# Optimization experiments

Measured on AMD Instinct MI355X. Metric: run time of the kernel, lower is better.

Reference implementation:

```python
import jax, jax.numpy as jnp
import numpy as np

H, I, E, TOPK = 2048, 1408, 8, 2
B, S = 2, 2048


def setup_inputs() -> dict:
    key = jax.random.key(0)
    k1, k2, k3, k4, k5 = jax.random.split(key, 5)
    x = jax.random.normal(k1, (B, S, H), dtype=jnp.float32)
    expert_indices = jax.random.randint(k2, (B, S, TOPK), 0, E, dtype=jnp.int64)
    expert_weights = jax.random.uniform(k3, (B, S, TOPK), dtype=jnp.float32)
    # params: w13 = concat([gate, up], dim=1) -> [E, 2I, H]; down_proj [E, H, I]
    w13 = jax.random.normal(k4, (E, 2 * I, H), dtype=jnp.float32) * 0.02
    down_proj = jax.random.normal(k5, (E, H, I), dtype=jnp.float32) * 0.02
    return {"x": x, "expert_indices": expert_indices, "expert_weights": expert_weights,
            "w13": w13, "down_proj": down_proj}


def _moe(x, expert_indices, expert_weights, w13, down_proj):
    b, s, h = x.shape
    T = b * s
    x_flat = x.reshape(T, h)
    idx = expert_indices.reshape(T, -1)            # [T, top_k]
    wts = expert_weights.reshape(T, -1)            # [T, top_k]
    # dense combine weights: routing[t, e] = sum of weights of slots routed to e
    # (matches original scatter/index_add combine, including duplicate experts)
    routing = jnp.zeros((T, w13.shape[0]), x.dtype).at[
        jnp.arange(T)[:, None], idx].add(wts)      # [T, E]
    # per-expert SwiGLU MLP computed densely, zeroed out by routing weights
    gu = jnp.einsum('th,eih->tei', x_flat, w13)    # [T, E, 2I]
    g, u = jnp.split(gu, 2, axis=-1)
    hact = jax.nn.silu(g) * u                      # [T, E, I]
    y = jnp.einsum('tei,ehi->teh', hact, down_proj)  # [T, E, H]
    out = jnp.einsum('te,teh->th', routing, y)     # [T, H]
    return out.reshape(b, s, h)


def reference(x, expert_indices, expert_weights, w13, down_proj):
    return _moe(x, expert_indices, expert_weights, w13, down_proj)
```

## Files before the change

### kernel.cpp

```cpp
#include <hip/hip_runtime.h>
#include <hip/hip_bf16.h>


typedef __bf16 bf16;
typedef bf16 bf16x8 __attribute__((ext_vector_type(8)));
typedef float f32x4 __attribute__((ext_vector_type(4)));

constexpr int Hdim = 2048;
constexpr int Idim = 1408;
constexpr int NE = 8;
constexpr int TOPK = 2;
constexpr int NT = 4096;
constexpr int NPAIR = 8192;
constexpr int BK = 64;

#define GLOAD16(G, L) __builtin_amdgcn_global_load_lds(                    \
    (const __attribute__((address_space(1))) void*)(G),                    \
    (__attribute__((address_space(3))) void*)(L), 16, 0, 0)


__global__ void k_cvt(const float* __restrict__ src, bf16* __restrict__ dst, int n8) {
    int i = blockIdx.x * 256 + threadIdx.x;
    if (i >= n8) return;
    f32x4 a = *reinterpret_cast<const f32x4*>(src + (size_t)i * 8);
    f32x4 b = *reinterpret_cast<const f32x4*>(src + (size_t)i * 8 + 4);
    bf16x8 v;
#pragma unroll
    for (int j = 0; j < 4; j++) { v[j] = (bf16)a[j]; v[4 + j] = (bf16)b[j]; }
    *reinterpret_cast<bf16x8*>(dst + (size_t)i * 8) = v;
}


__global__ void k_bin1(const int* __restrict__ eidx, int* __restrict__ chunkhist) {
    __shared__ int h[NE];
    int t = threadIdx.x;
    if (t < NE) h[t] = 0;
    __syncthreads();
    int p = blockIdx.x * 256 + t;
    atomicAdd(&h[eidx[p]], 1);
    __syncthreads();
    if (t < NE) chunkhist[blockIdx.x * NE + t] = h[t];
}

__global__ void k_bin2(int* __restrict__ meta, const int* __restrict__ chunkhist,
                       int* __restrict__ chunkbase) {
    if (threadIdx.x == 0) {
        int counts[NE];
        for (int e = 0; e < NE; e++) counts[e] = 0;
        for (int b = 0; b < 32; b++)
            for (int e = 0; e < NE; e++) {
                chunkbase[b * NE + e] = counts[e];
                counts[e] += chunkhist[b * NE + e];
            }
        int acc = 0;
        for (int e = 0; e < NE; e++) {
            meta[e] = counts[e];
            meta[8 + e] = acc;
            acc += counts[e];
        }
    }
}

__global__ void k_bin3(const int* __restrict__ eidx, const float* __restrict__ wts,
                       const int* __restrict__ meta, const int* __restrict__ chunkbase,
                       int* __restrict__ token_id, float* __restrict__ weightv) {
    __shared__ int earr[256];
    int t = threadIdx.x;
    int p = blockIdx.x * 256 + t;
    int e = eidx[p];
    earr[t] = e;
    __syncthreads();
    int rank = 0;
    for (int q = 0; q < t; q++) rank += (earr[q] == e) ? 1 : 0;
    int pos = meta[8 + e] + chunkbase[blockIdx.x * NE + e] + rank;
    token_id[pos] = p / TOPK;
    weightv[pos] = wts[p];
}


__global__ __launch_bounds__(256, 2) void k_gemm1(
    const bf16* __restrict__ xb, const bf16* __restrict__ w13b,
    const int* __restrict__ meta, bf16* __restrict__ hact) {
    const int flat = blockIdx.x;
    const int work = (flat & 7) * 176 + (flat >> 3);
    const int mslot = work & 15;
    const int grp = work >> 4;
    const int e = grp / 11;
    const int ytile = grp - e * 11;

    const int n_e = meta[e];
    const int m0 = mslot * 128;
    if (m0 >= n_e) return;
    const int base = meta[8 + e];
    const int* toks = (const int*)(meta + 64) + base;
    const bf16* wg = w13b + (size_t)e * (2 * Idim) * Hdim + (size_t)(ytile * 128) * Hdim;
    const bf16* wu = wg + (size_t)Idim * Hdim;

    __shared__ bf16 As[128 * 64];
    __shared__ bf16 Bg[128 * 64];
    __shared__ bf16 Bu[128 * 64];

    const int tid = threadIdx.x;
    const int lane = tid & 63;
    const int wid = tid >> 6;
    const int wr = wid >> 1, wc = wid & 1;
    const int l16 = lane & 15, lq = lane >> 4;

    const bf16* gA[4];
    const bf16* gG[4];
    const bf16* gU[4];
    int lo[4];
#pragma unroll
    for (int r = 0; r < 4; r++) {
        int sid = r * 256 + tid;
        int row = sid >> 3, seg = sid & 7;
        int ss = seg ^ (row & 7);
        lo[r] = (r * 256 + (tid & ~63)) * 16;
        int rr = m0 + row;
        if (rr >= n_e) rr = n_e - 1;
        gA[r] = xb + (size_t)toks[rr] * Hdim + ss * 8;
        gG[r] = wg + (size_t)row * Hdim + ss * 8;
        gU[r] = wu + (size_t)row * Hdim + ss * 8;
    }

    f32x4 accg[4][4], accu[4][4];
#pragma unroll
    for (int m = 0; m < 4; m++)
#pragma unroll
        for (int n = 0; n < 4; n++) {
            accg[m][n] = f32x4{0.f, 0.f, 0.f, 0.f};
            accu[m][n] = f32x4{0.f, 0.f, 0.f, 0.f};
        }

    for (int k0 = 0; k0 < Hdim; k0 += BK) {
        __syncthreads();
#pragma unroll
        for (int r = 0; r < 4; r++) {
            GLOAD16(gA[r] + k0, (char*)As + lo[r]);
            GLOAD16(gG[r] + k0, (char*)Bg + lo[r]);
            GLOAD16(gU[r] + k0, (char*)Bu + lo[r]);
        }
        __syncthreads();
#pragma unroll
        for (int kk = 0; kk < 2; ++kk) {
            bf16x8 af[4], bgf[4], buf_[4];
#pragma unroll
            for (int m = 0; m < 4; m++) {
                int row = wr * 64 + m * 16 + l16;
                int s = (kk * 4 + lq) ^ (row & 7);
                af[m] = *reinterpret_cast<const bf16x8*>(&As[row * 64 + s * 8]);
            }
#pragma unroll
            for (int n = 0; n < 4; n++) {
                int row = wc * 64 + n * 16 + l16;
                int s = (kk * 4 + lq) ^ (row & 7);
                bgf[n] = *reinterpret_cast<const bf16x8*>(&Bg[row * 64 + s * 8]);
                buf_[n] = *reinterpret_cast<const bf16x8*>(&Bu[row * 64 + s * 8]);
            }
#pragma unroll
            for (int m = 0; m < 4; m++)
#pragma unroll
                for (int n = 0; n < 4; n++) {
                    accg[m][n] = __builtin_amdgcn_mfma_f32_16x16x32_bf16(af[m], bgf[n], accg[m][n], 0, 0, 0);
                    accu[m][n] = __builtin_amdgcn_mfma_f32_16x16x32_bf16(af[m], buf_[n], accu[m][n], 0, 0, 0);
                }
        }
    }

    const int colbase = ytile * 128 + wc * 64;
#pragma unroll
    for (int m = 0; m < 4; m++) {
        int lr0 = m0 + wr * 64 + m * 16 + lq * 4;
#pragma unroll
        for (int j = 0; j < 4; j++) {
            int lr = lr0 + j;
            if (lr < n_e) {
                size_t rowoff = (size_t)(base + lr) * Idim;
#pragma unroll
                for (int n = 0; n < 4; n++) {
                    float g = accg[m][n][j], u = accu[m][n][j];
                    float v = (g / (1.f + __expf(-g))) * u;
                    hact[rowoff + colbase + n * 16 + l16] = (bf16)v;
                }
            }
        }
    }
}


__global__ __launch_bounds__(256, 2) void k_gemm2(
    const bf16* __restrict__ hact, const bf16* __restrict__ dpb,
    const int* __restrict__ meta, const float* __restrict__ weightv,
    float* __restrict__ out) {
    const int flat = blockIdx.x;
    const int work = (flat & 7) * 256 + (flat >> 3);
    const int mslot = work & 15;
    const int grp = work >> 4;
    const int e = grp >> 4;
    const int ytile = grp & 15;

    const int n_e = meta[e];
    const int m0 = mslot * 128;
    if (m0 >= n_e) return;
    const int base = meta[8 + e];
    const int* toks = (const int*)(meta + 64) + base;
    const bf16* wb = dpb + (size_t)e * Hdim * Idim + (size_t)(ytile * 128) * Idim;

    __shared__ bf16 As[128 * 64];
    __shared__ bf16 Bs[128 * 64];

    const int tid = threadIdx.x;
    const int lane = tid & 63;
    const int wid = tid >> 6;
    const int wr = wid >> 1, wc = wid & 1;
    const int l16 = lane & 15, lq = lane >> 4;

    const bf16* gA[4];
    const bf16* gB[4];
    int lo[4];
#pragma unroll
    for (int r = 0; r < 4; r++) {
        int sid = r * 256 + tid;
        int row = sid >> 3, seg = sid & 7;
        int ss = seg ^ (row & 7);
        lo[r] = (r * 256 + (tid & ~63)) * 16;
        int rr = m0 + row;
        if (rr >= n_e) rr = n_e - 1;
        gA[r] = hact + (size_t)(base + rr) * Idim + ss * 8;
        gB[r] = wb + (size_t)row * Idim + ss * 8;
    }

    f32x4 acc[4][4];
#pragma unroll
    for (int m = 0; m < 4; m++)
#pragma unroll
        for (int n = 0; n < 4; n++) acc[m][n] = f32x4{0.f, 0.f, 0.f, 0.f};

    for (int k0 = 0; k0 < Idim; k0 += BK) {
        __syncthreads();
#pragma unroll
        for (int r = 0; r < 4; r++) {
            GLOAD16(gA[r] + k0, (char*)As + lo[r]);
            GLOAD16(gB[r] + k0, (char*)Bs + lo[r]);
        }
        __syncthreads();
#pragma unroll
        for (int kk = 0; kk < 2; ++kk) {
            bf16x8 af[4], bf_[4];
#pragma unroll
            for (int m = 0; m < 4; m++) {
                int row = wr * 64 + m * 16 + l16;
                int s = (kk * 4 + lq) ^ (row & 7);
                af[m] = *reinterpret_cast<const bf16x8*>(&As[row * 64 + s * 8]);
            }
#pragma unroll
            for (int n = 0; n < 4; n++) {
                int row = wc * 64 + n * 16 + l16;
                int s = (kk * 4 + lq) ^ (row & 7);
                bf_[n] = *reinterpret_cast<const bf16x8*>(&Bs[row * 64 + s * 8]);
            }
#pragma unroll
            for (int m = 0; m < 4; m++)
#pragma unroll
                for (int n = 0; n < 4; n++)
                    acc[m][n] = __builtin_amdgcn_mfma_f32_16x16x32_bf16(af[m], bf_[n], acc[m][n], 0, 0, 0);
        }
    }

    const int colbase = ytile * 128 + wc * 64;
#pragma unroll
    for (int m = 0; m < 4; m++) {
        int lr0 = m0 + wr * 64 + m * 16 + lq * 4;
#pragma unroll
        for (int j = 0; j < 4; j++) {
            int lr = lr0 + j;
            if (lr < n_e) {
                int tok = toks[lr];
                float w = weightv[base + lr];
#pragma unroll
                for (int n = 0; n < 4; n++) {
                    float v = acc[m][n][j] * w;
                    unsafeAtomicAdd(&out[(size_t)tok * Hdim + colbase + n * 16 + l16], v);
                }
            }
        }
    }
}


extern "C" void kernel_launch(void* const* d_in, const int* in_sizes, int n_in,
                              void* d_out, int out_size, void* d_ws, size_t ws_size,
                              hipStream_t stream) {
    const float* x = (const float*)d_in[0];
    const int* eidx = (const int*)d_in[1];
    const float* ewts = (const float*)d_in[2];
    const float* w13 = (const float*)d_in[3];
    const float* dproj = (const float*)d_in[4];
    float* out = (float*)d_out;

    char* ws = (char*)d_ws;
    int* meta = (int*)ws;
    int* token_id = meta + 64;
    float* weightv = (float*)(meta + 64 + NPAIR);
    int* chunkhist = meta + 64 + 2 * NPAIR;
    int* chunkbase = chunkhist + 256;
    bf16* xb = (bf16*)(ws + 67840);
    bf16* w13b = xb + (size_t)NT * Hdim;
    bf16* dpb = w13b + (size_t)NE * 2 * Idim * Hdim;
    bf16* hact = dpb + (size_t)NE * Hdim * Idim;

    hipMemsetAsync(d_out, 0, (size_t)out_size * sizeof(float), stream);

    const int nx8 = NT * Hdim / 8;
    const int nw8 = NE * 2 * Idim * Hdim / 8;
    const int nd8 = NE * Hdim * Idim / 8;
    k_cvt<<<(nx8 + 255) / 256, 256, 0, stream>>>(x, xb, nx8);
    k_cvt<<<(nw8 + 255) / 256, 256, 0, stream>>>(w13, w13b, nw8);
    k_cvt<<<(nd8 + 255) / 256, 256, 0, stream>>>(dproj, dpb, nd8);

    k_bin1<<<32, 256, 0, stream>>>(eidx, chunkhist);
    k_bin2<<<1, 64, 0, stream>>>(meta, chunkhist, chunkbase);
    k_bin3<<<32, 256, 0, stream>>>(eidx, ewts, meta, chunkbase, token_id, weightv);

    k_gemm1<<<1408, 256, 0, stream>>>(xb, w13b, meta, hact);
    k_gemm2<<<2048, 256, 0, stream>>>(hact, dpb, meta, weightv, out);
}
```

Baseline: 351.8 us.

## Double-buffer LDS tiles in down-projection GEMM to overlap loads with MFMA

The second grouped GEMM (down projection) now uses two LDS buffer pairs. It issues the global-to-LDS loads for the next K tile before computing on the current one, so there is one barrier per tile instead of two. This aims to hide global load latency behind MFMA work. It doubles LDS use per block to 64KB, which could limit occupancy with two blocks per CU, and it relies on the barrier waiting for the async LDS loads to finish.

Result: slower. 359.3 us (+2.1%).

```diff
diff --git a/kernel.cpp b/kernel.cpp
--- a/kernel.cpp
+++ b/kernel.cpp
@@ -206,8 +206,10 @@
     const int* toks = (const int*)(meta + 64) + base;
     const bf16* wb = dpb + (size_t)e * Hdim * Idim + (size_t)(ytile * 128) * Idim;
 
-    __shared__ bf16 As[128 * 64];
-    __shared__ bf16 Bs[128 * 64];
+    __shared__ bf16 A0[128 * 64];
+    __shared__ bf16 B0[128 * 64];
+    __shared__ bf16 A1[128 * 64];
+    __shared__ bf16 B1[128 * 64];
 
     const int tid = threadIdx.x;
     const int lane = tid & 63;
@@ -236,35 +238,49 @@
 #pragma unroll
         for (int n = 0; n < 4; n++) acc[m][n] = f32x4{0.f, 0.f, 0.f, 0.f};
 
-    for (int k0 = 0; k0 < Idim; k0 += BK) {
+#define STG2(AB, BB, K0)                                                    \
+    {                                                                       \
+        _Pragma("unroll")                                                   \
+        for (int r = 0; r < 4; r++) {                                       \
+            GLOAD16(gA[r] + (K0), (char*)(AB) + lo[r]);                     \
+            GLOAD16(gB[r] + (K0), (char*)(BB) + lo[r]);                     \
+        }                                                                   \
+    }
+
+#define CMP2(AB, BB)                                                        \
+    {                                                                       \
+        _Pragma("unroll")                                                   \
+        for (int kk = 0; kk < 2; ++kk) {                                    \
+            bf16x8 af[4], bf_[4];                                           \
+            _Pragma("unroll")                                               \
+            for (int m = 0; m < 4; m++) {                                   \
+                int row = wr * 64 + m * 16 + l16;                           \
+                int s = (kk * 4 + lq) ^ (row & 7);                          \
+                af[m] = *reinterpret_cast<const bf16x8*>(&(AB)[row * 64 + s * 8]); \
+            }                                                               \
+            _Pragma("unroll")                                               \
+            for (int n = 0; n < 4; n++) {                                   \
+                int row = wc * 64 + n * 16 + l16;                           \
+                int s = (kk * 4 + lq) ^ (row & 7);                          \
+                bf_[n] = *reinterpret_cast<const bf16x8*>(&(BB)[row * 64 + s * 8]); \
+            }                                                               \
+            _Pragma("unroll")                                               \
+            for (int m = 0; m < 4; m++)                                     \
+                _Pragma("unroll")                                           \
+                for (int n = 0; n < 4; n++)                                 \
+                    acc[m][n] = __builtin_amdgcn_mfma_f32_16x16x32_bf16(af[m], bf_[n], acc[m][n], 0, 0, 0); \
+        }                                                                   \
+    }
+
+    STG2(A0, B0, 0);
+    __syncthreads();
+    for (int t = 0; t < Idim / BK; t += 2) {
+        STG2(A1, B1, (t + 1) * BK);
+        CMP2(A0, B0);
         __syncthreads();
-#pragma unroll
-        for (int r = 0; r < 4; r++) {
-            GLOAD16(gA[r] + k0, (char*)As + lo[r]);
-            GLOAD16(gB[r] + k0, (char*)Bs + lo[r]);
-        }
+        if (t + 2 < Idim / BK) STG2(A0, B0, (t + 2) * BK);
+        CMP2(A1, B1);
         __syncthreads();
-#pragma unroll
-        for (int kk = 0; kk < 2; ++kk) {
-            bf16x8 af[4], bf_[4];
-#pragma unroll
-            for (int m = 0; m < 4; m++) {
-                int row = wr * 64 + m * 16 + l16;
-                int s = (kk * 4 + lq) ^ (row & 7);
-                af[m] = *reinterpret_cast<const bf16x8*>(&As[row * 64 + s * 8]);
-            }
-#pragma unroll
-            for (int n = 0; n < 4; n++) {
-                int row = wc * 64 + n * 16 + l16;
-                int s = (kk * 4 + lq) ^ (row & 7);
-                bf_[n] = *reinterpret_cast<const bf16x8*>(&Bs[row * 64 + s * 8]);
-            }
-#pragma unroll
-            for (int m = 0; m < 4; m++)
-#pragma unroll
-                for (int n = 0; n < 4; n++)
-                    acc[m][n] = __builtin_amdgcn_mfma_f32_16x16x32_bf16(af[m], bf_[n], acc[m][n], 0, 0, 0);
-        }
     }
 
     const int colbase = ytile * 128 + wc * 64;
@@ -285,6 +301,8 @@
             }
         }
     }
+#undef STG2
+#undef CMP2
 }
 
 
```
